# Kernel optimization log

Measured on AMD Instinct MI355X. Metric: run time of the kernel, lower is better.

The kernel has to match this reference:

```python
import jax, jax.numpy as jnp
import numpy as np

B, N, C, H = 2, 2048, 768, 12
D = C // H
EPS = 1e-5


def setup_inputs() -> dict:
    key = jax.random.key(0)
    ks = jax.random.split(key, 12)
    s = 0.02
    return {
        "x": jax.random.normal(ks[0], (B, N, C), jnp.float32),
        "attn_mask": jax.random.randint(ks[1], (N, N), 0, 2) > 0,  # True = NOT allowed
        "ln1_g": jnp.ones((C,), jnp.float32),
        "ln1_b": jnp.zeros((C,), jnp.float32),
        "w_qkv": jax.random.normal(ks[2], (C, 3 * C), jnp.float32) * s,  # [in,out]
        "b_qkv": jnp.zeros((3 * C,), jnp.float32),
        "w_proj": jax.random.normal(ks[3], (C, C), jnp.float32) * s,
        "b_proj": jnp.zeros((C,), jnp.float32),
        "ls1": jnp.full((C,), 1e-5, jnp.float32),
        "ln2_g": jnp.ones((C,), jnp.float32),
        "ln2_b": jnp.zeros((C,), jnp.float32),
        "w1": jax.random.normal(ks[4], (C, 4 * C), jnp.float32) * s,
        "b1": jnp.zeros((4 * C,), jnp.float32),
        "w2": jax.random.normal(ks[5], (4 * C, C), jnp.float32) * s,
        "b2": jnp.zeros((C,), jnp.float32),
        "ls2": jnp.full((C,), 1e-5, jnp.float32),
    }


def layer_norm(x, g, b):
    mu = jnp.mean(x, axis=-1, keepdims=True)
    var = jnp.var(x, axis=-1, keepdims=True)
    return (x - mu) * jax.lax.rsqrt(var + EPS) * g + b


def reference(x, attn_mask, ln1_g, ln1_b, w_qkv, b_qkv, w_proj, b_proj, ls1,
              ln2_g, ln2_b, w1, b1, w2, b2, ls2):
    # ---- attention branch ----
    h = layer_norm(x, ln1_g, ln1_b)
    qkv = h @ w_qkv + b_qkv                       # [B,N,3C]
    qkv = qkv.reshape(B, N, 3, H, D).transpose(2, 0, 3, 1, 4)  # [3,B,H,N,D]
    q, k, v = qkv[0], qkv[1], qkv[2]
    scores = jnp.einsum('bhnd,bhmd->bhnm', q, k) * (D ** -0.5)  # [B,H,N,N]
    neg = jnp.finfo(scores.dtype).min
    scores = jnp.where(attn_mask, neg, scores)    # mask broadcasts over B,H
    attn = jax.nn.softmax(scores, axis=-1)
    o = jnp.einsum('bhnm,bhmd->bhnd', attn, v).transpose(0, 2, 1, 3).reshape(B, N, C)
    x = x + (o @ w_proj + b_proj) * ls1
    # ---- MLP branch ----
    h = layer_norm(x, ln2_g, ln2_b)
    h = jax.nn.gelu(h @ w1 + b1, approximate=False)
    x = x + (h @ w2 + b2) * ls2
    return x
```

## Files before the change

### kernel.cpp

```cpp
#include <hip/hip_runtime.h>
#include <hip/hip_bf16.h>
#include <math.h>

#define BN 2
#define SEQ 2048
#define CH 768
#define NH 12
#define HD 64
#define TOK (BN*SEQ)


using bf16_t = __hip_bfloat16;
typedef __attribute__((ext_vector_type(8))) short short8;
typedef __attribute__((ext_vector_type(8))) unsigned short ushort8;
typedef __attribute__((ext_vector_type(4))) float floatx4;
typedef __attribute__((ext_vector_type(2))) unsigned uintx2;

#define OFF_LN1G 0
#define OFF_LN1B 768
#define OFF_BQKV 1536
#define OFF_BPROJ 3840
#define OFF_LS1 4608
#define OFF_LN2G 5376
#define OFF_LN2B 6144
#define OFF_B1 6912
#define OFF_B2 9984
#define OFF_LS2 10752

__device__ inline float b2f(bf16_t v){ return __bfloat162float(v); }
__device__ inline bf16_t f2b(float v){ return __float2bfloat16(v); }
__device__ inline short f2bs(float v){ bf16_t b = __float2bfloat16(v); return *reinterpret_cast<short*>(&b); }
__device__ inline unsigned pk2(float a, float b){
  return (unsigned)(unsigned short)f2bs(a) | ((unsigned)(unsigned short)f2bs(b) << 16);
}
__device__ inline float sane(float v){ return (fabsf(v) < 1e30f) ? v : 0.0f; }
__device__ inline float clampf(float v, float lim){
  v = sane(v);
  return fminf(fmaxf(v, -lim), lim);
}
__device__ inline float ldf(const bf16_t* p){ return __bfloat162float(*p); }
__device__ inline float ldf(const float* p){ return *p; }
__device__ inline bool bf16_mode(const void* gref){
  return *reinterpret_cast<const unsigned*>(gref) == 0x3F803F80u;
}
__device__ inline void gload16(const void* g, void* l){
  __builtin_amdgcn_global_load_lds(
      (const __attribute__((address_space(1))) unsigned int*)g,
      (__attribute__((address_space(3))) unsigned int*)l, 16, 0, 0);
}

template<typename T>
__device__ inline void tr32(const T* __restrict__ src, size_t colOff, int stride,
    bf16_t* __restrict__ dst, int dstStride, int r0, int c0, float* smem, int tid)
{
  const int tx = tid & 31, ty = tid >> 5;
  #pragma unroll
  for (int j = 0; j < 4; j++)
    smem[(ty + j*8)*33 + tx] = ldf(src + (size_t)(r0 + ty + j*8) * stride + colOff + c0 + tx);
  __syncthreads();
  #pragma unroll
  for (int j = 0; j < 4; j++)
    dst[(size_t)(c0 + ty + j*8) * dstStride + r0 + tx] = f2b(smem[tx*33 + ty + j*8]);
}

template<typename T, bool GUARDED>
__global__ __launch_bounds__(256) void prep1_kernel(
    const T* __restrict__ x, const T* __restrict__ w_qkv, const T* __restrict__ w_proj,
    const T* __restrict__ w1, const T* __restrict__ w2,
    const T* __restrict__ g1, const T* __restrict__ b1_, const T* __restrict__ bqkv,
    const T* __restrict__ bproj, const T* __restrict__ ls1, const T* __restrict__ g2,
    const T* __restrict__ b2_, const T* __restrict__ bb1, const T* __restrict__ bb2,
    const T* __restrict__ ls2, const void* __restrict__ mask,
    float* __restrict__ pb, bf16_t* __restrict__ wqkvT, bf16_t* __restrict__ wprojT,
    unsigned long long* __restrict__ m1, bf16_t* __restrict__ a1,
    bf16_t* __restrict__ w1T, bf16_t* __restrict__ w2T,
    const void* __restrict__ gref)
{
  if (GUARDED && (bf16_mode(gref) != (sizeof(T) == 2))) return;
  __shared__ float smem[1056];
  const int tid = threadIdx.x;
  int wg = blockIdx.x;

  if (wg < 4096) {
    const T* xr = x + (size_t)wg * CH;
    float v0 = sane(ldf(xr + tid)), v1 = sane(ldf(xr + tid + 256)), v2 = sane(ldf(xr + tid + 512));
    float s  = v0 + v1 + v2;
    float s2 = v0*v0 + v1*v1 + v2*v2;
    #pragma unroll
    for (int o = 32; o > 0; o >>= 1) { s += __shfl_down(s, o, 64); s2 += __shfl_down(s2, o, 64); }
    if ((tid & 63) == 0) { smem[tid >> 6] = s; smem[(tid >> 6) + 4] = s2; }
    __syncthreads();
    if (tid == 0) {
      float ts = smem[0] + smem[1] + smem[2] + smem[3];
      float tq = smem[4] + smem[5] + smem[6] + smem[7];
      float mu = ts * (1.f / CH);
      float var = tq * (1.f / CH) - mu * mu;
      smem[8] = mu; smem[9] = rsqrtf(fmaxf(var, 0.f) + 1e-5f);
    }
    __syncthreads();
    const float mu = smem[8], rs = smem[9];
    bf16_t* orow = a1 + (size_t)wg * CH;
    orow[tid      ] = f2b(clampf((v0 - mu) * rs * ldf(g1 + tid      ) + ldf(b1_ + tid      ), 32.f));
    orow[tid + 256] = f2b(clampf((v1 - mu) * rs * ldf(g1 + tid + 256) + ldf(b1_ + tid + 256), 32.f));
    orow[tid + 512] = f2b(clampf((v2 - mu) * rs * ldf(g1 + tid + 512) + ldf(b1_ + tid + 512), 32.f));
    return;
  }
  wg -= 4096;
  if (wg < 1728) {
    tr32(w_qkv, 0, 2304, wqkvT, 768, (wg / 72) * 32, (wg % 72) * 32, smem, tid);
    return;
  }
  wg -= 1728;
  if (wg < 576) {
    tr32(w_proj, 0, 768, wprojT, 768, (wg / 24) * 32, (wg % 24) * 32, smem, tid);
    return;
  }
  wg -= 576;
  if (wg < 512) {
    const unsigned* mw = (const unsigned*)mask;
    unsigned accu = 0;
    #pragma unroll 8
    for (int i = 0; i < 64; i++) accu |= mw[i];
    const bool is8 = (accu > 1u);
    const int wave = tid >> 6, lane = tid & 63;
    #pragma unroll 4
    for (int i = 0; i < 32; i++) {
      const int word = wg * 128 + wave * 32 + i;
      const size_t elem = (size_t)word * 64 + lane;
      bool pred;
      if (is8) pred = ((const unsigned char*)mask)[elem] != 0;
      else     pred = ((const int*)mask)[elem] != 0;
      unsigned long long bits = __ballot(pred);
      if (lane == 0) m1[word] = bits;
    }
    return;
  }
  wg -= 512;
  if (wg < 1) {
    #define PCOPY(off, src, n) for (int i = tid; i < (n); i += 256) pb[(off)+i] = ldf((src)+i);
    PCOPY(OFF_LN1G, g1, 768)
    PCOPY(OFF_LN1B, b1_, 768)
    PCOPY(OFF_BQKV, bqkv, 2304)
    PCOPY(OFF_BPROJ, bproj, 768)
    PCOPY(OFF_LS1, ls1, 768)
    PCOPY(OFF_LN2G, g2, 768)
    PCOPY(OFF_LN2B, b2_, 768)
    PCOPY(OFF_B1, bb1, 3072)
    PCOPY(OFF_B2, bb2, 768)
    PCOPY(OFF_LS2, ls2, 768)
    #undef PCOPY
    return;
  }
  wg -= 1;
  if (wg < 2304) {
    tr32(w1, 0, 3072, w1T, 768, (wg / 96) * 32, (wg % 96) * 32, smem, tid);
    return;
  }
  wg -= 2304;
  {
    tr32(w2, 0, 768, w2T, 3072, (wg / 24) * 32, (wg % 24) * 32, smem, tid);
    return;
  }
}

template<typename T, bool GUARDED>
__global__ __launch_bounds__(256) void trc_kernel(const T* __restrict__ w1,
    const T* __restrict__ w2, bf16_t* __restrict__ w1Tc, bf16_t* __restrict__ w2Tc,
    int kc, const void* __restrict__ gref)
{
  if (GUARDED && (bf16_mode(gref) != (sizeof(T) == 2))) return;
  __shared__ float smem[1056];
  const int tid = threadIdx.x;
  int wg = blockIdx.x;
  if (wg < 576) {
    tr32(w1, (size_t)kc * 768, 3072, w1Tc, 768, (wg / 24) * 32, (wg % 24) * 32, smem, tid);
  } else {
    wg -= 576;
    tr32(w2 + (size_t)kc * 768 * 768, 0, 768, w2Tc, 768, (wg / 24) * 32, (wg % 24) * 32, smem, tid);
  }
}

__global__ __launch_bounds__(256) void ln2x_kernel(const bf16_t* __restrict__ x1,
    bf16_t* __restrict__ a2, const float* __restrict__ pb)
{
  __shared__ float red[10];
  const int row = blockIdx.x, tid = threadIdx.x;
  const bf16_t* xr = x1 + (size_t)row * CH;
  float v0 = sane(ldf(xr + tid)), v1 = sane(ldf(xr + tid + 256)), v2 = sane(ldf(xr + tid + 512));
  float s  = v0 + v1 + v2;
  float s2 = v0*v0 + v1*v1 + v2*v2;
  #pragma unroll
  for (int o = 32; o > 0; o >>= 1) { s += __shfl_down(s, o, 64); s2 += __shfl_down(s2, o, 64); }
  if ((tid & 63) == 0) { red[tid >> 6] = s; red[(tid >> 6) + 4] = s2; }
  __syncthreads();
  if (tid == 0) {
    float ts = red[0] + red[1] + red[2] + red[3];
    float tq = red[4] + red[5] + red[6] + red[7];
    float mu = ts * (1.f / CH);
    float var = tq * (1.f / CH) - mu * mu;
    red[8] = mu; red[9] = rsqrtf(fmaxf(var, 0.f) + 1e-5f);
  }
  __syncthreads();
  const float mu = red[8], rs = red[9];
  bf16_t* orow = a2 + (size_t)row * CH;
  orow[tid      ] = f2b(clampf((v0 - mu) * rs * pb[OFF_LN2G + tid      ] + pb[OFF_LN2B + tid      ], 32.f));
  orow[tid + 256] = f2b(clampf((v1 - mu) * rs * pb[OFF_LN2G + tid + 256] + pb[OFF_LN2B + tid + 256], 32.f));
  orow[tid + 512] = f2b(clampf((v2 - mu) * rs * pb[OFF_LN2G + tid + 512] + pb[OFF_LN2B + tid + 512], 32.f));
}

template<int MODE, int MT, int NT>
__global__ __launch_bounds__(256) void mgemm(
    const bf16_t* __restrict__ A, const bf16_t* __restrict__ BT,
    const float* __restrict__ pb, const int K, const int ldb,
    const int biasOff, const int scaleOff,
    const void* __restrict__ resid, const void* __restrict__ gref,
    bf16_t* __restrict__ o0, bf16_t* __restrict__ o1, bf16_t* __restrict__ vtout,
    float* __restrict__ oF, const bf16_t* __restrict__ stg,
    const int addPrev, const int finalize)
{
  constexpr int MI = MT / 32;
  constexpr int NI = NT / 32;
  __shared__ __align__(16) short As[2][MT * 32];
  __shared__ __align__(16) short Bs[2][NT * 32];
  const int tid = threadIdx.x;
  const int wave = tid >> 6, lane = tid & 63, lane15 = lane & 15, quad = lane >> 4;
  const int wr = (wave >> 1) * (MT / 2), wc = (wave & 1) * (NT / 2);
  const int mBase = blockIdx.y * MT;
  const int nBase = blockIdx.x * NT;

  floatx4 acc[MI][NI];
  #pragma unroll
  for (int mi = 0; mi < MI; mi++)
    #pragma unroll
    for (int ni = 0; ni < NI; ni++) acc[mi][ni] = (floatx4){0.f, 0.f, 0.f, 0.f};

  const bf16_t* aS0 = A  + (size_t)(mBase + (tid >> 2)) * K + (tid & 3) * 8;
  const bf16_t* aS1 = aS0 + (size_t)64 * K;
  const bf16_t* bS0 = BT + (size_t)(nBase + (tid >> 2)) * ldb + (tid & 3) * 8;
  const bf16_t* bS1 = bS0 + (size_t)64 * ldb;
  const int wfl = __builtin_amdgcn_readfirstlane(wave);
  short* aD0 = &As[0][wfl * 512];
  short* aD1 = (MT == 128) ? &As[0][2048 + wfl * 512] : nullptr;
  short* bD0 = &Bs[0][wfl * 512];
  short* bD1 = (NT == 128) ? &Bs[0][2048 + wfl * 512] : nullptr;

  auto STAGE = [&](int buf, int k0) {
    const int ab = buf * (MT * 32), bb = buf * (NT * 32);
    gload16(aS0 + k0, aD0 + ab);
    if (MT == 128) gload16(aS1 + k0, aD1 + ab);
    gload16(bS0 + k0, bD0 + bb);
    if (NT == 128) gload16(bS1 + k0, bD1 + bb);
  };

  const int nsteps = K / 32;
  int cur = 0;
  STAGE(0, 0);
  asm volatile("s_waitcnt vmcnt(0)" ::: "memory");
  __builtin_amdgcn_s_barrier();
  for (int t = 0; t < nsteps; ++t) {
    if (t + 1 < nsteps) STAGE(cur ^ 1, (t + 1) * 32);
    short8 av[MI], bv[NI];
    #pragma unroll
    for (int mi = 0; mi < MI; mi++)
      av[mi] = *(const short8*)&As[cur][(wr + mi * 16 + lane15) * 32 + quad * 8];
    #pragma unroll
    for (int ni = 0; ni < NI; ni++)
      bv[ni] = *(const short8*)&Bs[cur][(wc + ni * 16 + lane15) * 32 + quad * 8];
    #pragma unroll
    for (int mi = 0; mi < MI; mi++)
      #pragma unroll
      for (int ni = 0; ni < NI; ni++)
        acc[mi][ni] = __builtin_amdgcn_mfma_f32_16x16x32_bf16(av[mi], bv[ni], acc[mi][ni], 0, 0, 0);
    if (t + 1 < nsteps) {
      asm volatile("s_waitcnt vmcnt(0)" ::: "memory");
      __builtin_amdgcn_s_barrier();
      cur ^= 1;
    }
  }

  const bool rbf = (MODE == 1) ? bf16_mode(gref) : false;
  #pragma unroll
  for (int mi = 0; mi < MI; mi++) {
    #pragma unroll
    for (int ni = 0; ni < NI; ni++) {
      const int c0u = nBase + wc + ni * 16;
      const int col = c0u + lane15;
      float bia = 0.f, sc = 0.f;
      if (MODE == 0 || MODE == 1 || MODE == 2) bia = pb[biasOff + col];
      if (MODE == 1) sc = pb[scaleOff + col];
      if (MODE == 3 && finalize) { bia = pb[biasOff + col]; sc = pb[scaleOff + col]; }
      if (MODE == 0 && c0u >= 2 * CH) {
        const int cv = col - 2 * CH;
        const int bh = (mBase >> 11) * NH + (cv >> 6);
        const int d = cv & 63;
        const int tok0 = (mBase + wr + mi * 16 + quad * 4) & (SEQ - 1);
        float tv[4];
        #pragma unroll
        for (int r = 0; r < 4; r++) tv[r] = clampf(acc[mi][ni][r] + bia, 20.f);
        uintx2 pk = (uintx2){ pk2(tv[0], tv[1]), pk2(tv[2], tv[3]) };
        *(uintx2*)(vtout + ((size_t)(bh * 64 + d)) * SEQ + tok0) = pk;
        continue;
      }
      #pragma unroll
      for (int r = 0; r < 4; r++) {
        const int row = mBase + wr + mi * 16 + quad * 4 + r;
        float v = acc[mi][ni][r];
        if (MODE == 0) {
          const float cv = clampf(v + bia, 20.f);
          if (col < CH) o0[(size_t)row * CH + col] = f2b(cv * 0.125f);
          else          o1[(size_t)row * CH + (col - CH)] = f2b(cv);
        } else if (MODE == 1) {
          const size_t ix = (size_t)row * CH + col;
          const float rx = rbf ? b2f(((const bf16_t*)resid)[ix]) : ((const float*)resid)[ix];
          const bf16_t xv = f2b(rx + clampf(sc * (v + bia), 0.5f));
          o0[ix] = xv;
          o1[ix] = xv;
        } else if (MODE == 2) {
          const float h = v + bia;
          const float g = 0.5f * h * (1.f + erff(h * 0.70710678118f));
          o0[(size_t)row * CH + col] = f2b(clampf(g, 50.f));
        } else {
          const size_t ix = (size_t)row * CH + col;
          if (addPrev) v += oF[ix];
          if (!finalize) oF[ix] = v;
          else oF[ix] = b2f(stg[ix]) + clampf(sc * (v + bia), 0.5f);
        }
      }
    }
  }
}

__global__ __launch_bounds__(256) void attn6_kernel(bf16_t* __restrict__ q,
    const bf16_t* __restrict__ kbuf, const bf16_t* __restrict__ vtb,
    const unsigned long long* __restrict__ m1)
{
  __shared__ __align__(16) short Ks[2][64 * 72];
  __shared__ __align__(16) short Vs[2][64 * 72];
  __shared__ unsigned Plds[4][32 * 17];
  const int bh = blockIdx.y, b = bh / NH, h = bh % NH;
  const int q0 = blockIdx.x * 64;
  const int tid = threadIdx.x;
  const int wave = tid >> 6, l15 = tid & 15, quad = (tid & 63) >> 4;
  const int srow = tid >> 2, scc = (tid & 3) * 16;
  const size_t kgbase = (size_t)(b * SEQ) * CH + h * HD;
  const size_t vgbase = (size_t)(bh * HD) * SEQ;
  const int qrow = q0 + wave * 16 + l15;

  short8 qf[2];
  {
    const unsigned short* qp = (const unsigned short*)q
        + (size_t)(b * SEQ + qrow) * CH + h * HD + quad * 8;
    qf[0] = *(const short8*)(qp);
    qf[1] = *(const short8*)(qp + 32);
  }
  const unsigned long long* mrow = m1 + (size_t)qrow * (SEQ / 64);

  float mreg = -1.1e4f, lreg = 0.f;
  floatx4 oacc[4] = {{0,0,0,0},{0,0,0,0},{0,0,0,0},{0,0,0,0}};
  unsigned* pw = &Plds[wave][0];

  const unsigned short* kp0 = (const unsigned short*)kbuf + kgbase + (size_t)srow * CH + scc;
  const unsigned short* vp0 = (const unsigned short*)vtb + vgbase + (size_t)srow * SEQ + scc;

  {
    ushort8 k0r = *(const ushort8*)(kp0);
    ushort8 k1r = *(const ushort8*)(kp0 + 8);
    ushort8 v0r = *(const ushort8*)(vp0);
    ushort8 v1r = *(const ushort8*)(vp0 + 8);
    *(ushort8*)&Ks[0][srow * 72 + scc]     = k0r;
    *(ushort8*)&Ks[0][srow * 72 + scc + 8] = k1r;
    *(ushort8*)&Vs[0][srow * 72 + scc]     = v0r;
    *(ushort8*)&Vs[0][srow * 72 + scc + 8] = v1r;
  }
  __syncthreads();

  int cur = 0;
  ushort8 kr0, kr1, vr0, vr1;
  for (int k0 = 0; k0 < SEQ; k0 += 64) {
    const bool more = (k0 + 64 < SEQ);
    if (more) {
      const unsigned short* kp = kp0 + (size_t)(k0 + 64) * CH;
      const unsigned short* vp = vp0 + (k0 + 64);
      kr0 = *(const ushort8*)(kp);
      kr1 = *(const ushort8*)(kp + 8);
      vr0 = *(const ushort8*)(vp);
      vr1 = *(const ushort8*)(vp + 8);
    }

    const unsigned long long mw = mrow[k0 >> 6];
    float sv[4][4];
    float tmax = -1.0e30f;
    #pragma unroll
    for (int kb = 0; kb < 4; kb++) {
      floatx4 t = {0,0,0,0};
      short8 kf0 = *(const short8*)&Ks[cur][(kb * 16 + l15) * 72 + quad * 8];
      short8 kf1 = *(const short8*)&Ks[cur][(kb * 16 + l15) * 72 + 32 + quad * 8];
      __builtin_amdgcn_s_setprio(1);
      t = __builtin_amdgcn_mfma_f32_16x16x32_bf16(kf0, qf[0], t, 0, 0, 0);
      t = __builtin_amdgcn_mfma_f32_16x16x32_bf16(kf1, qf[1], t, 0, 0, 0);
      __builtin_amdgcn_s_setprio(0);
      #pragma unroll
      for (int r = 0; r < 4; r++) {
        float v = t[r];
        if ((mw >> (kb * 16 + quad * 4 + r)) & 1ull) v = -1.0e30f;
        sv[kb][r] = v;
        tmax = fmaxf(tmax, v);
      }
    }
    tmax = fmaxf(tmax, __shfl_xor(tmax, 16, 64));
    tmax = fmaxf(tmax, __shfl_xor(tmax, 32, 64));

    if (__any(tmax > mreg)) {
      const float mnew = fmaxf(mreg, tmax);
      float alpha = __expf(mreg - mnew);
      alpha = (alpha <= 1.f) ? alpha : 0.f;
      lreg *= alpha;
      #pragma unroll
      for (int db = 0; db < 4; db++)
        #pragma unroll
        for (int r = 0; r < 4; r++) oacc[db][r] *= alpha;
      mreg = mnew;
    }

    float ls = 0.f;
    #pragma unroll
    for (int kb = 0; kb < 4; kb++) {
      float pr[4];
      #pragma unroll
      for (int r = 0; r < 4; r++) {
        const float pv = __expf(sv[kb][r] - mreg);
        pr[r] = pv;
        ls += pv;
      }
      pw[(8 * kb + 2 * quad)     * 17 + l15] = pk2(pr[0], pr[1]);
      pw[(8 * kb + 2 * quad + 1) * 17 + l15] = pk2(pr[2], pr[3]);
    }
    ls += __shfl_xor(ls, 16, 64);
    ls += __shfl_xor(ls, 32, 64);
    lreg += ls;

    #pragma unroll
    for (int s = 0; s < 2; s++) {
      union { unsigned u[4]; short8 s8; } pu;
      #pragma unroll
      for (int w = 0; w < 4; w++)
        pu.u[w] = pw[(16 * s + 4 * quad + w) * 17 + l15];
      __builtin_amdgcn_s_setprio(1);
      #pragma unroll
      for (int db = 0; db < 4; db++) {
        short8 vf = *(const short8*)&Vs[cur][(db * 16 + l15) * 72 + s * 32 + quad * 8];
        oacc[db] = __builtin_amdgcn_mfma_f32_16x16x32_bf16(vf, pu.s8, oacc[db], 0, 0, 0);
      }
      __builtin_amdgcn_s_setprio(0);
    }

    if (more) {
      *(ushort8*)&Ks[cur ^ 1][srow * 72 + scc]     = kr0;
      *(ushort8*)&Ks[cur ^ 1][srow * 72 + scc + 8] = kr1;
      *(ushort8*)&Vs[cur ^ 1][srow * 72 + scc]     = vr0;
      *(ushort8*)&Vs[cur ^ 1][srow * 72 + scc + 8] = vr1;
      __syncthreads();
      cur ^= 1;
    }
  }

  const float inv = 1.f / fmaxf(lreg, 1e-20f);
  unsigned short* op = (unsigned short*)q
      + (size_t)(b * SEQ + qrow) * CH + h * HD + quad * 4;
  #pragma unroll
  for (int db = 0; db < 4; db++) {
    const unsigned lo = pk2(clampf(oacc[db][0] * inv, 10.f), clampf(oacc[db][1] * inv, 10.f));
    const unsigned hi = pk2(clampf(oacc[db][2] * inv, 10.f), clampf(oacc[db][3] * inv, 10.f));
    *(uintx2*)(op + db * 16) = (uintx2){lo, hi};
  }
}

extern "C" void kernel_launch(void* const* d_in, const int* in_sizes, int n_in,
                              void* d_out, int out_size, void* d_ws, size_t ws_size,
                              hipStream_t stream) {
  const void* x      = d_in[0];
  const void* mask   = d_in[1];
  const void* ln1_g  = d_in[2];
  const void* ln1_b  = d_in[3];
  const void* w_qkv  = d_in[4];
  const void* b_qkv  = d_in[5];
  const void* w_proj = d_in[6];
  const void* b_proj = d_in[7];
  const void* ls1    = d_in[8];
  const void* ln2_g  = d_in[9];
  const void* ln2_b  = d_in[10];
  const void* w1     = d_in[11];
  const void* b1     = d_in[12];
  const void* w2     = d_in[13];
  const void* b2     = d_in[14];
  const void* ls2    = d_in[15];
  const void* gref   = ln1_g;

  char* ws = (char*)d_ws;
  float*  pb     = (float*)ws;
  bf16_t* a12    = (bf16_t*)(ws + 65536);
  bf16_t* vt     = (bf16_t*)(ws + 65536 + 6291456);
  bf16_t* stage  = vt;
  char*   r3     = ws + 65536 + 2 * 6291456;
  bf16_t* wqkvT  = (bf16_t*)r3;
  bf16_t* wprojT = (bf16_t*)(r3 + 3538944);
  bf16_t* hact   = (bf16_t*)r3;
  char*   r4     = ws + 65536 + 3 * 6291456;
  unsigned long long* mi1 = (unsigned long long*)r4;
  bf16_t* w1Tc   = (bf16_t*)r4;
  bf16_t* w2Tc   = (bf16_t*)(r4 + 1179648);
  char*   r5     = ws + 21299200;
  bf16_t* w1T    = (bf16_t*)r5;
  bf16_t* w2T    = (bf16_t*)(r5 + 4718592);
  bf16_t* dQ     = (bf16_t*)d_out;
  bf16_t* dK     = dQ + 3145728;
  float*  outF   = (float*)d_out;

  const long long xs = in_sizes ? (long long)in_sizes[0] : 0;
  const int mode = (xs == 6291456LL) ? 1 : (xs == 12582912LL ? 2 : 0);
  const bool doFull = (ws_size >= 30736384ULL);
  const int prepGrid = doFull ? 11521 : 6913;

  #define PREP_ARGS(T) (const T*)x, (const T*)w_qkv, (const T*)w_proj, (const T*)w1, (const T*)w2, \
      (const T*)ln1_g, (const T*)ln1_b, (const T*)b_qkv, (const T*)b_proj, (const T*)ls1, \
      (const T*)ln2_g, (const T*)ln2_b, (const T*)b1, (const T*)b2, (const T*)ls2, \
      mask, pb, wqkvT, wprojT, mi1, a12, w1T, w2T, gref
  if (mode == 1)      prep1_kernel<bf16_t, false><<<prepGrid, 256, 0, stream>>>(PREP_ARGS(bf16_t));
  else if (mode == 2) prep1_kernel<float,  false><<<prepGrid, 256, 0, stream>>>(PREP_ARGS(float));
  else {
    prep1_kernel<bf16_t, true><<<prepGrid, 256, 0, stream>>>(PREP_ARGS(bf16_t));
    prep1_kernel<float,  true><<<prepGrid, 256, 0, stream>>>(PREP_ARGS(float));
  }
  #undef PREP_ARGS

  mgemm<0, 128, 128><<<dim3(18, 32), 256, 0, stream>>>(a12, wqkvT, pb, 768, 768, OFF_BQKV, 0,
      nullptr, gref, dQ, dK, vt, nullptr, nullptr, 0, 0);
  attn6_kernel<<<dim3(SEQ / 64, BN * NH), 256, 0, stream>>>(dQ, dK, vt, mi1);
  mgemm<1, 64, 64><<<dim3(12, 64), 256, 0, stream>>>(dQ, wprojT, pb, 768, 768, OFF_BPROJ, OFF_LS1,
      x, gref, dK, stage, nullptr, nullptr, nullptr, 0, 0);
  ln2x_kernel<<<TOK, 256, 0, stream>>>(dK, a12, pb);
  for (int kc = 0; kc < 4; kc++) {
    const bf16_t* bt1; const bf16_t* bt2; int ldb2;
    if (doFull) {
      bt1 = w1T + (size_t)kc * 768 * 768;
      bt2 = w2T + (size_t)kc * 768;
      ldb2 = 3072;
    } else {
      if (mode == 1)      trc_kernel<bf16_t, false><<<1152, 256, 0, stream>>>((const bf16_t*)w1, (const bf16_t*)w2, w1Tc, w2Tc, kc, gref);
      else if (mode == 2) trc_kernel<float,  false><<<1152, 256, 0, stream>>>((const float*)w1,  (const float*)w2,  w1Tc, w2Tc, kc, gref);
      else {
        trc_kernel<bf16_t, true><<<1152, 256, 0, stream>>>((const bf16_t*)w1, (const bf16_t*)w2, w1Tc, w2Tc, kc, gref);
        trc_kernel<float,  true><<<1152, 256, 0, stream>>>((const float*)w1,  (const float*)w2,  w1Tc, w2Tc, kc, gref);
      }
      bt1 = w1Tc; bt2 = w2Tc; ldb2 = 768;
    }
    mgemm<2, 64, 64><<<dim3(12, 64), 256, 0, stream>>>(a12, bt1, pb, 768, 768, OFF_B1 + kc * 768, 0,
        nullptr, gref, hact, nullptr, nullptr, nullptr, nullptr, 0, 0);
    mgemm<3, 64, 64><<<dim3(12, 64), 256, 0, stream>>>(hact, bt2, pb, 768, ldb2, OFF_B2, OFF_LS2,
        nullptr, gref, nullptr, nullptr, nullptr, outF, stage, kc > 0 ? 1 : 0, kc == 3 ? 1 : 0);
  }
}
```

Before: 419.1 us.

## Swizzle GEMM block order, use hardware bf16 pack, compact workspace layout

Remaps the GEMM workgroup index so consecutive blocks are spread in groups of eight, likely to spread work across the MI355X's XCDs and improve L2 reuse. The attention kernel computes the row max as a tree per key block and replaces software bf16 packing with the v_cvt_pk_bf16_f32 instruction. The workspace is also repacked: the mask moves next to the projection weights and the full transposed MLP weights reuse an earlier region. This lowers the workspace threshold needed for the full-weight path. The packing instruction may round differently from the old conversion, and the swizzle assumes the block count divides by eight.

```diff
diff --git a/kernel.cpp b/kernel.cpp
--- a/kernel.cpp
+++ b/kernel.cpp
@@ -32,6 +32,11 @@
 __device__ inline short f2bs(float v){ bf16_t b = __float2bfloat16(v); return *reinterpret_cast<short*>(&b); }
 __device__ inline unsigned pk2(float a, float b){
   return (unsigned)(unsigned short)f2bs(a) | ((unsigned)(unsigned short)f2bs(b) << 16);
+}
+__device__ inline unsigned cvtpk(float a, float b){
+  unsigned r;
+  asm("v_cvt_pk_bf16_f32 %0, %1, %2" : "=v"(r) : "v"(a), "v"(b));
+  return r;
 }
 __device__ inline float sane(float v){ return (fabsf(v) < 1e30f) ? v : 0.0f; }
 __device__ inline float clampf(float v, float lim){
@@ -225,8 +230,13 @@
   const int tid = threadIdx.x;
   const int wave = tid >> 6, lane = tid & 63, lane15 = lane & 15, quad = lane >> 4;
   const int wr = (wave >> 1) * (MT / 2), wc = (wave & 1) * (NT / 2);
-  const int mBase = blockIdx.y * MT;
-  const int nBase = blockIdx.x * NT;
+
+  int bflat = blockIdx.y * gridDim.x + blockIdx.x;
+  const int nwg = gridDim.x * gridDim.y;
+  bflat = (bflat & 7) * (nwg >> 3) + (bflat >> 3);
+  const int bX = bflat % gridDim.x, bY = bflat / gridDim.x;
+  const int mBase = bY * MT;
+  const int nBase = bX * NT;
 
   floatx4 acc[MI][NI];
   #pragma unroll
@@ -330,7 +340,7 @@
   }
 }
 
-__global__ __launch_bounds__(256) void attn6_kernel(bf16_t* __restrict__ q,
+__global__ __launch_bounds__(256) void attn7_kernel(bf16_t* __restrict__ q,
     const bf16_t* __restrict__ kbuf, const bf16_t* __restrict__ vtb,
     const unsigned long long* __restrict__ m1)
 {
@@ -389,7 +399,7 @@
 
     const unsigned long long mw = mrow[k0 >> 6];
     float sv[4][4];
-    float tmax = -1.0e30f;
+    float kbm[4];
     #pragma unroll
     for (int kb = 0; kb < 4; kb++) {
       floatx4 t = {0,0,0,0};
@@ -404,9 +414,10 @@
         float v = t[r];
         if ((mw >> (kb * 16 + quad * 4 + r)) & 1ull) v = -1.0e30f;
         sv[kb][r] = v;
-        tmax = fmaxf(tmax, v);
       }
-    }
+      kbm[kb] = fmaxf(fmaxf(fmaxf(sv[kb][0], sv[kb][1]), sv[kb][2]), sv[kb][3]);
+    }
+    float tmax = fmaxf(fmaxf(fmaxf(kbm[0], kbm[1]), kbm[2]), kbm[3]);
     tmax = fmaxf(tmax, __shfl_xor(tmax, 16, 64));
     tmax = fmaxf(tmax, __shfl_xor(tmax, 32, 64));
 
@@ -432,8 +443,8 @@
         pr[r] = pv;
         ls += pv;
       }
-      pw[(8 * kb + 2 * quad)     * 17 + l15] = pk2(pr[0], pr[1]);
-      pw[(8 * kb + 2 * quad + 1) * 17 + l15] = pk2(pr[2], pr[3]);
+      pw[(8 * kb + 2 * quad)     * 17 + l15] = cvtpk(pr[0], pr[1]);
+      pw[(8 * kb + 2 * quad + 1) * 17 + l15] = cvtpk(pr[2], pr[3]);
     }
     ls += __shfl_xor(ls, 16, 64);
     ls += __shfl_xor(ls, 32, 64);
@@ -504,21 +515,20 @@
   char*   r3     = ws + 65536 + 2 * 6291456;
   bf16_t* wqkvT  = (bf16_t*)r3;
   bf16_t* wprojT = (bf16_t*)(r3 + 3538944);
+  unsigned long long* mi1 = (unsigned long long*)(r3 + 4718592);
   bf16_t* hact   = (bf16_t*)r3;
   char*   r4     = ws + 65536 + 3 * 6291456;
-  unsigned long long* mi1 = (unsigned long long*)r4;
   bf16_t* w1Tc   = (bf16_t*)r4;
   bf16_t* w2Tc   = (bf16_t*)(r4 + 1179648);
-  char*   r5     = ws + 21299200;
-  bf16_t* w1T    = (bf16_t*)r5;
-  bf16_t* w2T    = (bf16_t*)(r5 + 4718592);
+  bf16_t* w1T    = (bf16_t*)r4;
+  bf16_t* w2T    = (bf16_t*)(r4 + 4718592);
   bf16_t* dQ     = (bf16_t*)d_out;
   bf16_t* dK     = dQ + 3145728;
   float*  outF   = (float*)d_out;
 
   const long long xs = in_sizes ? (long long)in_sizes[0] : 0;
   const int mode = (xs == 6291456LL) ? 1 : (xs == 12582912LL ? 2 : 0);
-  const bool doFull = (ws_size >= 30736384ULL);
+  const bool doFull = (ws_size >= 28377088ULL);
   const int prepGrid = doFull ? 11521 : 6913;
 
   #define PREP_ARGS(T) (const T*)x, (const T*)w_qkv, (const T*)w_proj, (const T*)w1, (const T*)w2, \
@@ -535,7 +545,7 @@
 
   mgemm<0, 128, 128><<<dim3(18, 32), 256, 0, stream>>>(a12, wqkvT, pb, 768, 768, OFF_BQKV, 0,
       nullptr, gref, dQ, dK, vt, nullptr, nullptr, 0, 0);
-  attn6_kernel<<<dim3(SEQ / 64, BN * NH), 256, 0, stream>>>(dQ, dK, vt, mi1);
+  attn7_kernel<<<dim3(SEQ / 64, BN * NH), 256, 0, stream>>>(dQ, dK, vt, mi1);
   mgemm<1, 64, 64><<<dim3(12, 64), 256, 0, stream>>>(dQ, wprojT, pb, 768, 768, OFF_BPROJ, OFF_LS1,
       x, gref, dK, stage, nullptr, nullptr, nullptr, 0, 0);
   ln2x_kernel<<<TOK, 256, 0, stream>>>(dK, a12, pb);
```

New measurement: 401.2 us. -4.3%, faster.
